# Kernel tuning notes

Hardware: AMD Instinct MI355X
Metric: run time of the kernel (lower is better)

## Reference

```python
import jax, jax.numpy as jnp
import numpy as np

DIM = 512
HEADS = 8
RES = 14
HEAD_DIM = DIM // HEADS
N = RES * RES


def _make_bias_idxs(res):
    pts = [(i, j) for i in range(res) for j in range(res)]
    offs = {}
    idxs = []
    for p1 in pts:
        for p2 in pts:
            o = (abs(p1[0] - p2[0]), abs(p1[1] - p2[1]))
            if o not in offs:
                offs[o] = len(offs)
            idxs.append(offs[o])
    return np.asarray(idxs, dtype=np.int32).reshape(res * res, res * res), len(offs)


def setup_inputs() -> dict:
    key = jax.random.key(0)
    ks = jax.random.split(key, 6)
    idxs, n_off = _make_bias_idxs(RES)  # n_off == 196 for res=14
    B = 128
    return {
        "x": jax.random.normal(ks[0], (B, DIM, RES, RES), dtype=jnp.float32),
        "qkv_w": jax.random.normal(ks[1], (3 * DIM, DIM), dtype=jnp.float32) * 0.02,
        "qkv_b": jnp.zeros((3 * DIM,), dtype=jnp.float32),
        "proj_w": jax.random.normal(ks[2], (DIM, DIM), dtype=jnp.float32) * 0.02,
        "proj_b": jnp.zeros((DIM,), dtype=jnp.float32),
        "attention_biases": jax.random.normal(ks[3], (HEADS, n_off), dtype=jnp.float32) * 0.02,
        "bias_idxs": jnp.asarray(idxs),
    }


def reference(x, qkv_w, qkv_b, proj_w, proj_b, attention_biases, bias_idxs):
    B, C, H, W = x.shape
    scale = HEAD_DIM ** -0.5
    # 1x1 conv == channel-wise linear
    qkv = jnp.einsum("oc,bchw->bohw", qkv_w, x) + qkv_b[None, :, None, None]
    q, k, v = jnp.split(qkv, 3, axis=1)
    # [B, heads, head_dim, N]
    q = q.reshape(B, HEADS, HEAD_DIM, N)
    k = k.reshape(B, HEADS, HEAD_DIM, N)
    v = v.reshape(B, HEADS, HEAD_DIM, N)
    attn = jnp.einsum("bhdn,bhdm->bhnm", q, k) * scale  # [B,h,N,N]
    bias = attention_biases[:, bias_idxs]  # gather -> [h,N,N]
    attn = jax.nn.softmax(attn + bias[None], axis=-1)
    out = jnp.einsum("bhnm,bhdm->bhdn", attn, v).reshape(B, C, H, W)
    return jnp.einsum("oc,bchw->bohw", proj_w, out) + proj_b[None, :, None, None]
```

## Files before the change

### kernel.cpp

```cpp
#include <hip/hip_runtime.h>
#include <hip/hip_bf16.h>
#include <math.h>

#define B_     128
#define DIM_   512
#define HEADS_ 8
#define HD_    64
#define N_     196
#define NP_    224
#define NROW_  208
#define SCALE_ 0.125f
#define BSTRIDE (DIM_ * N_)
#define J_     (B_ * NP_)

typedef unsigned short u16;
typedef unsigned int   u32;
typedef __attribute__((ext_vector_type(8))) short bf16x8;
typedef __attribute__((ext_vector_type(4))) float f32x4;

__device__ __forceinline__ u16 f2bf(float f) {
    u32 u = __float_as_uint(f);
    return (u16)((u + 0x7fffu + ((u >> 16) & 1u)) >> 16);
}
__device__ __forceinline__ void gload_lds16(const u16* g, u16* l) {
    __builtin_amdgcn_global_load_lds(
        (const __attribute__((address_space(1))) void*)g,
        (__attribute__((address_space(3))) void*)l, 16, 0, 0);
}


__global__ __launch_bounds__(256) void prep(
    const float* __restrict__ x, u16* __restrict__ XT,
    const float* __restrict__ qw, u16* __restrict__ qd,
    const float* __restrict__ pw, u16* __restrict__ pd,
    const float* __restrict__ biases, const int* __restrict__ bidx,
    float* __restrict__ EB)
{
    const int id = blockIdx.x;
    const int t = threadIdx.x;
    if (id < 4096) {
        __shared__ float tile[64][65];
        const int jj = t & 63, ii = t >> 6;
        const int ct = id & 7, ntb = (id >> 3) & 3, b = id >> 5;
        const float* xb = x + ((size_t)b * DIM_ + ct * 64) * N_;
        const int n0 = ntb * 64;
        #pragma unroll
        for (int s = 0; s < 16; ++s) {
            const int i = ii + s * 4;
            const int n = n0 + jj;
            tile[i][jj] = (n < N_) ? xb[(size_t)i * N_ + n] : 0.f;
        }
        __syncthreads();
        const int lo = t & 15, hi = t >> 4;
        const int c8 = hi & 7, ng = hi >> 3;
        #pragma unroll
        for (int s = 0; s < 2; ++s) {
            const int n_loc = (s * 2 + ng) * 16 + lo;
            const int nn = n0 + n_loc;
            if (nn < N_) {
                const int j = b * NP_ + nn;
                const int c0 = ct * 64 + c8 * 8;
                u16 vv[8];
                #pragma unroll
                for (int e = 0; e < 8; ++e) vv[e] = f2bf(tile[c8 * 8 + e][n_loc]);
                uint4 o;
                o.x = (u32)vv[0] | ((u32)vv[1] << 16);
                o.y = (u32)vv[2] | ((u32)vv[3] << 16);
                o.z = (u32)vv[4] | ((u32)vv[5] << 16);
                o.w = (u32)vv[6] | ((u32)vv[7] << 16);
                *reinterpret_cast<uint4*>(XT + (size_t)(j >> 4) * 8192
                    + (c0 >> 5) * 512 + ((c0 >> 3) & 3) * 128 + (j & 15) * 8) = o;
            }
        }
    } else if (id < 5760) {
        const int e = id - 4096;
        const int n = e % NROW_, h = e / NROW_;
        const int m = t;
        if (m < NP_) {
            float v = 0.f;
            if (n < N_ && m < N_) v = __expf(biases[h * N_ + bidx[n * N_ + m]]);
            EB[((size_t)h * NROW_ + n) * NP_ + m] = v;
        }
    } else {
        const bool pj = id >= 6144;
        const int cb = id - (pj ? 6144 : 5760);
        const float* src = pj ? pw : qw;
        u16* dst = pj ? pd : qd;
        const int nch = pj ? (DIM_ * DIM_ / 8) : (3 * DIM_ * DIM_ / 8);
        const int c = cb * 256 + t;
        if (c < nch) {
            const int m16 = c & 15, q = (c >> 4) & 3, kb = (c >> 6) & 15, mb = c >> 10;
            const float* s = src + (size_t)(mb * 16 + m16) * DIM_ + kb * 32 + q * 8;
            const float4 v0 = reinterpret_cast<const float4*>(s)[0];
            const float4 v1 = reinterpret_cast<const float4*>(s)[1];
            uint4 o;
            o.x = (u32)f2bf(v0.x) | ((u32)f2bf(v0.y) << 16);
            o.y = (u32)f2bf(v0.z) | ((u32)f2bf(v0.w) << 16);
            o.z = (u32)f2bf(v1.x) | ((u32)f2bf(v1.y) << 16);
            o.w = (u32)f2bf(v1.z) | ((u32)f2bf(v1.w) << 16);
            reinterpret_cast<uint4*>(dst)[c] = o;
        }
    }
}

template<bool QKV>
__global__ __launch_bounds__(256) void gemmF(
    const u16* __restrict__ Bt, const u16* __restrict__ W,
    const float* __restrict__ bias,
    u16* __restrict__ o_q, u16* __restrict__ o_k, u16* __restrict__ o_v,
    float* __restrict__ o_f)
{
    __shared__ u16 Bs[2][8192];
    const int t = threadIdx.x;
    const int wave = t >> 6, lane = t & 63;
    const int m16 = lane & 15, quad = lane >> 4;

    constexpr int MT  = QKV ? 12 : 4;
    constexpr int NWG = (J_ / 128) * MT;
    const int bid = blockIdx.x;
    const int swz = (bid & 7) * (NWG / 8) + (bid >> 3);
    const int mt = swz % MT;
    const int jt = swz / MT;
    const int m0 = mt * 128, j0 = jt * 128;
    const int wy = wave >> 1, wx = wave & 1;

    const u16* gBb = Bt + (size_t)(jt * 8) * 8192;
    const u16* A2 = W + (size_t)(mt * 8 + wy * 4) * 8192 + quad * 128 + m16 * 8;

    const int roff = quad * 128 + m16 * 8;

    f32x4 acc[4][4];
    const f32x4 z4 = {0.f, 0.f, 0.f, 0.f};
    #pragma unroll
    for (int fi = 0; fi < 4; ++fi)
        #pragma unroll
        for (int fj = 0; fj < 4; ++fj) acc[fi][fj] = z4;

    #pragma unroll
    for (int c = 0; c < 4; ++c) {
        const int g = c * 256 + t;
        const int f = g >> 7, s = (g >> 6) & 1, ch = g & 63;
        gload_lds16(gBb + (size_t)f * 8192 + s * 512 + ch * 8, Bs[0] + g * 8);
    }
    for (int kt = 0; kt < 8; ++kt) {
        const int cur = kt & 1;
        __syncthreads();
        bf16x8 af[2][4];
        #pragma unroll
        for (int s = 0; s < 2; ++s)
            #pragma unroll
            for (int fi = 0; fi < 4; ++fi)
                af[s][fi] = *reinterpret_cast<const bf16x8*>(
                    A2 + (size_t)fi * 8192 + (kt * 2 + s) * 512);
        if (kt < 7) {
            #pragma unroll
            for (int c = 0; c < 4; ++c) {
                const int g = c * 256 + t;
                const int f = g >> 7, s = (g >> 6) & 1, ch = g & 63;
                gload_lds16(gBb + (size_t)f * 8192 + ((kt + 1) * 2 + s) * 512 + ch * 8, Bs[cur ^ 1] + g * 8);
            }
        }
        #pragma unroll
        for (int ks = 0; ks < 2; ++ks) {
            bf16x8 bf[4];
            #pragma unroll
            for (int fj = 0; fj < 4; ++fj)
                bf[fj] = *reinterpret_cast<const bf16x8*>(Bs[cur] + ((wx * 4 + fj) * 2 + ks) * 512 + roff);
            #pragma unroll
            for (int fi = 0; fi < 4; ++fi)
                #pragma unroll
                for (int fj = 0; fj < 4; ++fj)
                    acc[fi][fj] = __builtin_amdgcn_mfma_f32_16x16x32_bf16(af[ks][fi], bf[fj], acc[fi][fj], 0, 0, 0);
        }
    }

    const int mbase = m0 + wy * 64;
    float bb[4][4];
    #pragma unroll
    for (int fi = 0; fi < 4; ++fi)
        #pragma unroll
        for (int r = 0; r < 4; ++r) bb[fi][r] = bias[mbase + fi * 16 + quad * 4 + r];

    if (QKV) {
        const int part = mbase >> 9;
        const int h = (mbase & 511) >> 6;
        #pragma unroll
        for (int fj = 0; fj < 4; ++fj) {
            const int j = j0 + wx * 64 + fj * 16 + m16;
            const u32 b = (u32)j / 224u;
            const int n = j - (int)b * 224;
            if (part < 2) {
                u16* base = (part == 0 ? o_q : o_k) + (((size_t)b * HEADS_ + h) * NP_ + n) * HD_;
                #pragma unroll
                for (int fi = 0; fi < 4; ++fi) {
                    const int d0 = fi * 16 + quad * 4;
                    uint2 pk;
                    pk.x = (u32)f2bf(acc[fi][fj][0] + bb[fi][0]) | ((u32)f2bf(acc[fi][fj][1] + bb[fi][1]) << 16);
                    pk.y = (u32)f2bf(acc[fi][fj][2] + bb[fi][2]) | ((u32)f2bf(acc[fi][fj][3] + bb[fi][3]) << 16);
                    *reinterpret_cast<uint2*>(base + d0) = pk;
                }
            } else {
                u16* vb = o_v + (((size_t)b * HEADS_ + h) * HD_) * NP_ + n;
                #pragma unroll
                for (int fi = 0; fi < 4; ++fi) {
                    const int d0 = fi * 16 + quad * 4;
                    #pragma unroll
                    for (int r = 0; r < 4; ++r)
                        vb[(size_t)(d0 + r) * NP_] = f2bf(acc[fi][fj][r] + bb[fi][r]);
                }
            }
        }
    } else {
        #pragma unroll
        for (int fj = 0; fj < 4; ++fj) {
            const int j = j0 + wx * 64 + fj * 16 + m16;
            const u32 b = (u32)j / 224u;
            const int n = j - (int)b * 224;
            if (n < N_) {
                float* ob = o_f + (size_t)b * BSTRIDE + n;
                #pragma unroll
                for (int fi = 0; fi < 4; ++fi) {
                    const int r0 = mbase + fi * 16 + quad * 4;
                    #pragma unroll
                    for (int r = 0; r < 4; ++r)
                        ob[(size_t)(r0 + r) * N_] = acc[fi][fj][r] + bb[fi][r];
                }
            }
        }
    }
}

__global__ __launch_bounds__(512) void attn_mfma(
    const u16* __restrict__ qT, const u16* __restrict__ kT,
    const u16* __restrict__ vS, const float* __restrict__ EB,
    u16* __restrict__ OT)
{
    __shared__ u16 Ks[224 * 64];
    __shared__ u16 Vs[64 * 232];
    __shared__ u16 P[8][16 * 232];
    const int t = threadIdx.x;
    const int wave = t >> 6, lane = t & 63;
    const int m16 = lane & 15, quad = lane >> 4;
    const int b = blockIdx.x, h = blockIdx.y;
    const u16* qTb = qT + ((size_t)b * HEADS_ + h) * (NP_ * HD_);
    const u16* kTb = kT + ((size_t)b * HEADS_ + h) * (NP_ * HD_);
    const u16* vb  = vS + ((size_t)b * HEADS_ + h) * (HD_ * NP_);
    const float* ebh = EB + (size_t)h * NROW_ * NP_;
    u16* Pw = P[wave];
    const f32x4 z4 = {0.f, 0.f, 0.f, 0.f};

    #pragma unroll
    for (int i = 0; i < 4; ++i) {
        const int c = t + i * 512;
        if (c < 1792) {
            const int row = c >> 3, ch = c & 7;
            const bf16x8 d = *reinterpret_cast<const bf16x8*>(kTb + row * HD_ + ch * 8);
            *reinterpret_cast<bf16x8*>(Ks + row * 64 + ((ch ^ (row & 7)) * 8)) = d;
        }
    }
    #pragma unroll
    for (int i = 0; i < 4; ++i) {
        const int c = t + i * 512;
        if (c < 1792) {
            const u32 row = (u32)c / 28u;
            const int ch = c - (int)row * 28;
            const bf16x8 d = *reinterpret_cast<const bf16x8*>(vb + (size_t)row * NP_ + ch * 8);
            *reinterpret_cast<bf16x8*>(Vs + row * 232 + ch * 8) = d;
        }
    }
    __syncthreads();

    for (int nt = wave; nt < 13; nt += 8) {
        f32x4 s[14];
        #pragma unroll
        for (int mt = 0; mt < 14; ++mt) s[mt] = z4;
        #pragma unroll
        for (int ks = 0; ks < 2; ++ks) {
            const bf16x8 a = *reinterpret_cast<const bf16x8*>(
                qTb + (size_t)(nt * 16 + m16) * HD_ + ks * 32 + quad * 8);
            const int ch = ((ks * 4 + quad) ^ (m16 & 7)) * 8;
            #pragma unroll
            for (int mtile = 0; mtile < 14; ++mtile) {
                const bf16x8 bf = *reinterpret_cast<const bf16x8*>(
                    Ks + (mtile * 16 + m16) * 64 + ch);
                s[mtile] = __builtin_amdgcn_mfma_f32_16x16x32_bf16(a, bf, s[mtile], 0, 0, 0);
            }
        }
        float mx[4] = {-INFINITY, -INFINITY, -INFINITY, -INFINITY};
        #pragma unroll
        for (int mt = 0; mt < 14; ++mt)
            #pragma unroll
            for (int r = 0; r < 4; ++r) mx[r] = fmaxf(mx[r], s[mt][r]);
        #pragma unroll
        for (int off = 1; off < 16; off <<= 1)
            #pragma unroll
            for (int r = 0; r < 4; ++r) mx[r] = fmaxf(mx[r], __shfl_xor(mx[r], off, 64));
        #pragma unroll
        for (int r = 0; r < 4; ++r) mx[r] *= SCALE_;

        const float* ebn = ebh + (size_t)(nt * 16 + quad * 4) * NP_ + m16;
        float sum[4] = {0.f, 0.f, 0.f, 0.f};
        #pragma unroll
        for (int mt = 0; mt < 14; ++mt) {
            #pragma unroll
            for (int r = 0; r < 4; ++r) {
                const float e = __expf(fmaf(s[mt][r], SCALE_, -mx[r])) * ebn[(size_t)r * NP_ + mt * 16];
                s[mt][r] = e;
                sum[r] += e;
            }
        }
        #pragma unroll
        for (int off = 1; off < 16; off <<= 1)
            #pragma unroll
            for (int r = 0; r < 4; ++r) sum[r] += __shfl_xor(sum[r], off, 64);
        float inv[4];
        #pragma unroll
        for (int r = 0; r < 4; ++r) inv[r] = 1.f / sum[r];

        #pragma unroll
        for (int mt = 0; mt < 14; ++mt)
            #pragma unroll
            for (int r = 0; r < 4; ++r)
                Pw[(quad * 4 + r) * 232 + mt * 16 + m16] = f2bf(s[mt][r] * inv[r]);

        f32x4 o[4];
        #pragma unroll
        for (int dt = 0; dt < 4; ++dt) o[dt] = z4;
        #pragma unroll
        for (int ks = 0; ks < 7; ++ks) {
            const bf16x8 a = *reinterpret_cast<const bf16x8*>(Pw + m16 * 232 + ks * 32 + quad * 8);
            #pragma unroll
            for (int dt = 0; dt < 4; ++dt) {
                const bf16x8 bf = *reinterpret_cast<const bf16x8*>(
                    Vs + (dt * 16 + m16) * 232 + ks * 32 + quad * 8);
                o[dt] = __builtin_amdgcn_mfma_f32_16x16x32_bf16(a, bf, o[dt], 0, 0, 0);
            }
        }
        #pragma unroll
        for (int r = 0; r < 4; ++r) {
            const int n = nt * 16 + quad * 4 + r;
            if (n < N_) {
                const int j = b * NP_ + n;
                #pragma unroll
                for (int dt = 0; dt < 4; ++dt) {
                    const int c = h * HD_ + dt * 16 + m16;
                    OT[(size_t)(j >> 4) * 8192 + (c >> 5) * 512
                       + ((c >> 3) & 3) * 128 + (j & 15) * 8 + (c & 7)] = f2bf(o[dt][r]);
                }
            }
        }
    }
}

extern "C" void kernel_launch(void* const* d_in, const int* in_sizes, int n_in,
                              void* d_out, int out_size, void* d_ws, size_t ws_size,
                              hipStream_t stream) {
    const float* x      = (const float*)d_in[0];
    const float* qkv_w  = (const float*)d_in[1];
    const float* qkv_b  = (const float*)d_in[2];
    const float* proj_w = (const float*)d_in[3];
    const float* proj_b = (const float*)d_in[4];
    const float* biases = (const float*)d_in[5];
    const int*   bidx   = (const int*)d_in[6];
    float* out = (float*)d_out;

    char* w = (char*)d_ws;
    u16* XT  = (u16*)w; w += (size_t)B_ * NP_ * DIM_ * 2;
    u16* qTw = (u16*)w; w += (size_t)B_ * HEADS_ * NP_ * HD_ * 2;
    u16* vSw = (u16*)w; w += (size_t)B_ * HEADS_ * HD_ * NP_ * 2;
    float* EB = (float*)w; w += (size_t)HEADS_ * NROW_ * NP_ * 4;
    u16* wq  = (u16*)w; w += (size_t)3 * DIM_ * DIM_ * 2;
    u16* wpj = (u16*)w;
    u16* kTw = (u16*)d_out;

    prep<<<dim3(6272), 256, 0, stream>>>(x, XT, qkv_w, wq, proj_w, wpj, biases, bidx, EB);
    gemmF<true><<<dim3((J_ / 128) * 12), 256, 0, stream>>>(XT, wq, qkv_b, qTw, kTw, vSw, nullptr);
    attn_mfma<<<dim3(B_, HEADS_), 512, 0, stream>>>(qTw, kTw, vSw, EB, XT);
    gemmF<false><<<dim3((J_ / 128) * 4), 256, 0, stream>>>(XT, wpj, proj_b, nullptr, nullptr, nullptr, out);
}
```

Before: 277.8 us.

## Rewrite GEMMs as 256x256 tiles with 8 waves and 4-slot async LDS pipeline

Replaces the 128x128 tile GEMM (4 waves, B-only LDS double buffer, A read straight from global) with a 256x256 tile GEMM using 8 waves. Both A and B are staged into LDS through a 4-slot ring with explicit vmcnt waits and split barriers, plus s_setprio around the MFMA bursts. The aim is more reuse per tile and better overlap of global loads with MFMA work. In exchange it uses 128KB of LDS and more accumulator registers per thread, which lowers occupancy, and it launches fewer workgroups.

```diff
diff --git a/kernel.cpp b/kernel.cpp
--- a/kernel.cpp
+++ b/kernel.cpp
@@ -104,126 +104,176 @@
 }
 
 template<bool QKV>
-__global__ __launch_bounds__(256) void gemmF(
+__global__ __launch_bounds__(512) void gemm8(
     const u16* __restrict__ Bt, const u16* __restrict__ W,
     const float* __restrict__ bias,
     u16* __restrict__ o_q, u16* __restrict__ o_k, u16* __restrict__ o_v,
     float* __restrict__ o_f)
 {
-    __shared__ u16 Bs[2][8192];
+    __shared__ u16 S[4 * 16384];
     const int t = threadIdx.x;
     const int wave = t >> 6, lane = t & 63;
     const int m16 = lane & 15, quad = lane >> 4;
 
-    constexpr int MT  = QKV ? 12 : 4;
-    constexpr int NWG = (J_ / 128) * MT;
+    constexpr int MT  = QKV ? 6 : 2;
+    constexpr int NWG = (J_ / 256) * MT;
     const int bid = blockIdx.x;
     const int swz = (bid & 7) * (NWG / 8) + (bid >> 3);
     const int mt = swz % MT;
     const int jt = swz / MT;
-    const int m0 = mt * 128, j0 = jt * 128;
-    const int wy = wave >> 1, wx = wave & 1;
-
-    const u16* gBb = Bt + (size_t)(jt * 8) * 8192;
-    const u16* A2 = W + (size_t)(mt * 8 + wy * 4) * 8192 + quad * 128 + m16 * 8;
-
+    const int j0 = jt * 256;
+    const int wy = wave >> 2, wx = wave & 3;
+
+    const u16* gA = W  + (size_t)(mt * 16) * 8192;
+    const u16* gB = Bt + (size_t)(jt * 16) * 8192;
     const int roff = quad * 128 + m16 * 8;
 
-    f32x4 acc[4][4];
+    auto STAGE = [&](int h, int part) {
+        const int s = h & 1, ktt = h >> 1, slot = h & 3;
+        #pragma unroll
+        for (int i = 0; i < 2; ++i) {
+            const int g = t + 512 * (part * 2 + i);
+            const int isB = g >> 10;
+            const int fr = (g & 1023) >> 6, c = g & 63;
+            const u16* src = (isB ? gB : gA) + (size_t)fr * 8192 + (ktt * 2 + s) * 512 + c * 8;
+            gload_lds16(src, S + slot * 16384 + isB * 8192 + (g & 1023) * 8);
+        }
+    };
+
+    f32x4 acc[8][4];
     const f32x4 z4 = {0.f, 0.f, 0.f, 0.f};
     #pragma unroll
-    for (int fi = 0; fi < 4; ++fi)
+    for (int fi = 0; fi < 8; ++fi)
         #pragma unroll
         for (int fj = 0; fj < 4; ++fj) acc[fi][fj] = z4;
 
     #pragma unroll
-    for (int c = 0; c < 4; ++c) {
-        const int g = c * 256 + t;
-        const int f = g >> 7, s = (g >> 6) & 1, ch = g & 63;
-        gload_lds16(gBb + (size_t)f * 8192 + s * 512 + ch * 8, Bs[0] + g * 8);
-    }
+    for (int h = 0; h < 4; ++h) { STAGE(h, 0); STAGE(h, 1); }
+
+    #pragma unroll
     for (int kt = 0; kt < 8; ++kt) {
-        const int cur = kt & 1;
-        __syncthreads();
-        bf16x8 af[2][4];
-        #pragma unroll
-        for (int s = 0; s < 2; ++s)
-            #pragma unroll
-            for (int fi = 0; fi < 4; ++fi)
-                af[s][fi] = *reinterpret_cast<const bf16x8*>(
-                    A2 + (size_t)fi * 8192 + (kt * 2 + s) * 512);
-        if (kt < 7) {
-            #pragma unroll
-            for (int c = 0; c < 4; ++c) {
-                const int g = c * 256 + t;
-                const int f = g >> 7, s = (g >> 6) & 1, ch = g & 63;
-                gload_lds16(gBb + (size_t)f * 8192 + ((kt + 1) * 2 + s) * 512 + ch * 8, Bs[cur ^ 1] + g * 8);
-            }
-        }
-        #pragma unroll
-        for (int ks = 0; ks < 2; ++ks) {
-            bf16x8 bf[4];
-            #pragma unroll
-            for (int fj = 0; fj < 4; ++fj)
-                bf[fj] = *reinterpret_cast<const bf16x8*>(Bs[cur] + ((wx * 4 + fj) * 2 + ks) * 512 + roff);
-            #pragma unroll
-            for (int fi = 0; fi < 4; ++fi)
-                #pragma unroll
-                for (int fj = 0; fj < 4; ++fj)
-                    acc[fi][fj] = __builtin_amdgcn_mfma_f32_16x16x32_bf16(af[ks][fi], bf[fj], acc[fi][fj], 0, 0, 0);
-        }
-    }
-
-    const int mbase = m0 + wy * 64;
-    float bb[4][4];
-    #pragma unroll
-    for (int fi = 0; fi < 4; ++fi)
-        #pragma unroll
-        for (int r = 0; r < 4; ++r) bb[fi][r] = bias[mbase + fi * 16 + quad * 4 + r];
-
-    if (QKV) {
-        const int part = mbase >> 9;
-        const int h = (mbase & 511) >> 6;
-        #pragma unroll
-        for (int fj = 0; fj < 4; ++fj) {
-            const int j = j0 + wx * 64 + fj * 16 + m16;
-            const u32 b = (u32)j / 224u;
-            const int n = j - (int)b * 224;
-            if (part < 2) {
-                u16* base = (part == 0 ? o_q : o_k) + (((size_t)b * HEADS_ + h) * NP_ + n) * HD_;
-                #pragma unroll
-                for (int fi = 0; fi < 4; ++fi) {
-                    const int d0 = fi * 16 + quad * 4;
-                    uint2 pk;
-                    pk.x = (u32)f2bf(acc[fi][fj][0] + bb[fi][0]) | ((u32)f2bf(acc[fi][fj][1] + bb[fi][1]) << 16);
-                    pk.y = (u32)f2bf(acc[fi][fj][2] + bb[fi][2]) | ((u32)f2bf(acc[fi][fj][3] + bb[fi][3]) << 16);
-                    *reinterpret_cast<uint2*>(base + d0) = pk;
+        const int sA = (2 * kt) & 3, sB = (2 * kt + 1) & 3;
+        const bool doStage = (kt >= 1 && kt <= 6);
+        if (kt == 0) asm volatile("s_waitcnt vmcnt(12)" ::: "memory");
+        else         asm volatile("s_waitcnt vmcnt(4)"  ::: "memory");
+        __builtin_amdgcn_s_barrier();
+        if (doStage) STAGE(2 * kt + 2, 0);
+        {
+            bf16x8 af[8];
+            #pragma unroll
+            for (int fi = 0; fi < 8; ++fi)
+                af[fi] = *reinterpret_cast<const bf16x8*>(S + sA * 16384 + (wy * 8 + fi) * 512 + roff);
+            bf16x8 b0 = *reinterpret_cast<const bf16x8*>(S + sA * 16384 + 8192 + (wx * 4 + 0) * 512 + roff);
+            bf16x8 b1 = *reinterpret_cast<const bf16x8*>(S + sA * 16384 + 8192 + (wx * 4 + 1) * 512 + roff);
+            asm volatile("s_waitcnt lgkmcnt(0)" ::: "memory");
+            __builtin_amdgcn_s_setprio(1);
+            #pragma unroll
+            for (int fi = 0; fi < 8; ++fi) {
+                acc[fi][0] = __builtin_amdgcn_mfma_f32_16x16x32_bf16(af[fi], b0, acc[fi][0], 0, 0, 0);
+                acc[fi][1] = __builtin_amdgcn_mfma_f32_16x16x32_bf16(af[fi], b1, acc[fi][1], 0, 0, 0);
+            }
+            __builtin_amdgcn_s_setprio(0);
+            __builtin_amdgcn_s_barrier();
+            if (doStage) STAGE(2 * kt + 2, 1);
+            bf16x8 b2 = *reinterpret_cast<const bf16x8*>(S + sA * 16384 + 8192 + (wx * 4 + 2) * 512 + roff);
+            bf16x8 b3 = *reinterpret_cast<const bf16x8*>(S + sA * 16384 + 8192 + (wx * 4 + 3) * 512 + roff);
+            asm volatile("s_waitcnt lgkmcnt(0)" ::: "memory");
+            __builtin_amdgcn_s_setprio(1);
+            #pragma unroll
+            for (int fi = 0; fi < 8; ++fi) {
+                acc[fi][2] = __builtin_amdgcn_mfma_f32_16x16x32_bf16(af[fi], b2, acc[fi][2], 0, 0, 0);
+                acc[fi][3] = __builtin_amdgcn_mfma_f32_16x16x32_bf16(af[fi], b3, acc[fi][3], 0, 0, 0);
+            }
+            __builtin_amdgcn_s_setprio(0);
+        }
+        if (kt == 0)      asm volatile("s_waitcnt vmcnt(8)" ::: "memory");
+        else if (kt == 7) asm volatile("s_waitcnt vmcnt(0)" ::: "memory");
+        else              asm volatile("s_waitcnt vmcnt(4)" ::: "memory");
+        __builtin_amdgcn_s_barrier();
+        if (doStage) STAGE(2 * kt + 3, 0);
+        {
+            bf16x8 af[8];
+            #pragma unroll
+            for (int fi = 0; fi < 8; ++fi)
+                af[fi] = *reinterpret_cast<const bf16x8*>(S + sB * 16384 + (wy * 8 + fi) * 512 + roff);
+            bf16x8 b0 = *reinterpret_cast<const bf16x8*>(S + sB * 16384 + 8192 + (wx * 4 + 0) * 512 + roff);
+            bf16x8 b1 = *reinterpret_cast<const bf16x8*>(S + sB * 16384 + 8192 + (wx * 4 + 1) * 512 + roff);
+            asm volatile("s_waitcnt lgkmcnt(0)" ::: "memory");
+            __builtin_amdgcn_s_setprio(1);
+            #pragma unroll
+            for (int fi = 0; fi < 8; ++fi) {
+                acc[fi][0] = __builtin_amdgcn_mfma_f32_16x16x32_bf16(af[fi], b0, acc[fi][0], 0, 0, 0);
+                acc[fi][1] = __builtin_amdgcn_mfma_f32_16x16x32_bf16(af[fi], b1, acc[fi][1], 0, 0, 0);
+            }
+            __builtin_amdgcn_s_setprio(0);
+            __builtin_amdgcn_s_barrier();
+            if (doStage) STAGE(2 * kt + 3, 1);
+            bf16x8 b2 = *reinterpret_cast<const bf16x8*>(S + sB * 16384 + 8192 + (wx * 4 + 2) * 512 + roff);
+            bf16x8 b3 = *reinterpret_cast<const bf16x8*>(S + sB * 16384 + 8192 + (wx * 4 + 3) * 512 + roff);
+            asm volatile("s_waitcnt lgkmcnt(0)" ::: "memory");
+            __builtin_amdgcn_s_setprio(1);
+            #pragma unroll
+            for (int fi = 0; fi < 8; ++fi) {
+                acc[fi][2] = __builtin_amdgcn_mfma_f32_16x16x32_bf16(af[fi], b2, acc[fi][2], 0, 0, 0);
+                acc[fi][3] = __builtin_amdgcn_mfma_f32_16x16x32_bf16(af[fi], b3, acc[fi][3], 0, 0, 0);
+            }
+            __builtin_amdgcn_s_setprio(0);
+        }
+    }
+
+    #pragma unroll
+    for (int g = 0; g < 2; ++g) {
+        const int mbase = mt * 256 + wy * 128 + g * 64;
+        float bb[4][4];
+        #pragma unroll
+        for (int fi = 0; fi < 4; ++fi)
+            #pragma unroll
+            for (int r = 0; r < 4; ++r) bb[fi][r] = bias[mbase + fi * 16 + quad * 4 + r];
+
+        if (QKV) {
+            const int part = mbase >> 9;
+            const int h = (mbase & 511) >> 6;
+            #pragma unroll
+            for (int fj = 0; fj < 4; ++fj) {
+                const int j = j0 + wx * 64 + fj * 16 + m16;
+                const u32 b = (u32)j / 224u;
+                const int n = j - (int)b * 224;
+                if (part < 2) {
+                    u16* base = (part == 0 ? o_q : o_k) + (((size_t)b * HEADS_ + h) * NP_ + n) * HD_;
+                    #pragma unroll
+                    for (int fi = 0; fi < 4; ++fi) {
+                        const int d0 = fi * 16 + quad * 4;
+                        uint2 pk;
+                        pk.x = (u32)f2bf(acc[g * 4 + fi][fj][0] + bb[fi][0]) | ((u32)f2bf(acc[g * 4 + fi][fj][1] + bb[fi][1]) << 16);
+                        pk.y = (u32)f2bf(acc[g * 4 + fi][fj][2] + bb[fi][2]) | ((u32)f2bf(acc[g * 4 + fi][fj][3] + bb[fi][3]) << 16);
+                        *reinterpret_cast<uint2*>(base + d0) = pk;
+                    }
+                } else {
+                    u16* vb = o_v + (((size_t)b * HEADS_ + h) * HD_) * NP_ + n;
+                    #pragma unroll
+                    for (int fi = 0; fi < 4; ++fi) {
+                        const int d0 = fi * 16 + quad * 4;
+                        #pragma unroll
+                        for (int r = 0; r < 4; ++r)
+                            vb[(size_t)(d0 + r) * NP_] = f2bf(acc[g * 4 + fi][fj][r] + bb[fi][r]);
+                    }
                 }
-            } else {
-                u16* vb = o_v + (((size_t)b * HEADS_ + h) * HD_) * NP_ + n;
-                #pragma unroll
-                for (int fi = 0; fi < 4; ++fi) {
-                    const int d0 = fi * 16 + quad * 4;
+            }
+        } else {
+            #pragma unroll
+            for (int fj = 0; fj < 4; ++fj) {
+                const int j = j0 + wx * 64 + fj * 16 + m16;
+                const u32 b = (u32)j / 224u;
+                const int n = j - (int)b * 224;
+                if (n < N_) {
+                    float* ob = o_f + (size_t)b * BSTRIDE + n;
                     #pragma unroll
-                    for (int r = 0; r < 4; ++r)
-                        vb[(size_t)(d0 + r) * NP_] = f2bf(acc[fi][fj][r] + bb[fi][r]);
-                }
-            }
-        }
-    } else {
-        #pragma unroll
-        for (int fj = 0; fj < 4; ++fj) {
-            const int j = j0 + wx * 64 + fj * 16 + m16;
-            const u32 b = (u32)j / 224u;
-            const int n = j - (int)b * 224;
-            if (n < N_) {
-                float* ob = o_f + (size_t)b * BSTRIDE + n;
-                #pragma unroll
-                for (int fi = 0; fi < 4; ++fi) {
-                    const int r0 = mbase + fi * 16 + quad * 4;
-                    #pragma unroll
-                    for (int r = 0; r < 4; ++r)
-                        ob[(size_t)(r0 + r) * N_] = acc[fi][fj][r] + bb[fi][r];
+                    for (int fi = 0; fi < 4; ++fi) {
+                        const int r0 = mbase + fi * 16 + quad * 4;
+                        #pragma unroll
+                        for (int r = 0; r < 4; ++r)
+                            ob[(size_t)(r0 + r) * N_] = acc[g * 4 + fi][fj][r] + bb[fi][r];
+                    }
                 }
             }
         }
@@ -374,7 +424,7 @@
     u16* kTw = (u16*)d_out;
 
     prep<<<dim3(6272), 256, 0, stream>>>(x, XT, qkv_w, wq, proj_w, wpj, biases, bidx, EB);
-    gemmF<true><<<dim3((J_ / 128) * 12), 256, 0, stream>>>(XT, wq, qkv_b, qTw, kTw, vSw, nullptr);
+    gemm8<true><<<dim3((J_ / 256) * 6), 512, 0, stream>>>(XT, wq, qkv_b, qTw, kTw, vSw, nullptr);
     attn_mfma<<<dim3(B_, HEADS_), 512, 0, stream>>>(qTw, kTw, vSw, EB, XT);
-    gemmF<false><<<dim3((J_ / 128) * 4), 256, 0, stream>>>(XT, wpj, proj_b, nullptr, nullptr, nullptr, out);
-}
+    gemm8<false><<<dim3((J_ / 256) * 2), 512, 0, stream>>>(XT, wpj, proj_b, nullptr, nullptr, nullptr, out);
+}
```

Measured after the change: 258.1 us. 7.1% less time.
